# Performance work log

Hardware: AMD Instinct MI355X
Metric: run time of the kernel (lower is better)

## Reference

```python
import jax, jax.numpy as jnp
import numpy as np

B, C, H, W, K, NCLASS = 8, 512, 96, 96, 32, 19
EPS = 1e-5


def setup_inputs() -> dict:
    key = jax.random.key(0)
    ks = jax.random.split(key, 10)
    return {
        "x": jax.random.normal(ks[0], (B, C, H, W), dtype=jnp.float32),
        "conv_w": jax.random.normal(ks[1], (C, C), dtype=jnp.float32) * (1.0 / np.sqrt(C)),
        "bn2_w": jax.random.uniform(ks[2], (C,), dtype=jnp.float32, minval=0.5, maxval=1.5),
        "bn2_b": jax.random.normal(ks[3], (C,), dtype=jnp.float32) * 0.1,
        "bn2_mean": jnp.zeros((C,), jnp.float32),
        "bn2_var": jnp.ones((C,), jnp.float32),
        "codewords": jax.random.normal(ks[4], (K, C), dtype=jnp.float32) * (1.0 / np.sqrt(C)),
        "scale": jax.random.uniform(ks[5], (K,), dtype=jnp.float32, minval=-1.0, maxval=0.0),
        "bn1_w": jax.random.uniform(ks[6], (K,), dtype=jnp.float32, minval=0.5, maxval=1.5),
        "bn1_b": jax.random.normal(ks[7], (K,), dtype=jnp.float32) * 0.1,
        "bn1_mean": jnp.zeros((K,), jnp.float32),
        "bn1_var": jnp.ones((K,), jnp.float32),
        "fc_w": jax.random.normal(ks[8], (C, C), dtype=jnp.float32) * (1.0 / np.sqrt(C)),
        "fc_b": jnp.zeros((C,), jnp.float32),
        "se_w": jax.random.normal(ks[9], (NCLASS, C), dtype=jnp.float32) * (1.0 / np.sqrt(C)),
        "se_b": jnp.zeros((NCLASS,), jnp.float32),
    }


def reference(x, conv_w, bn2_w, bn2_b, bn2_mean, bn2_var,
              codewords, scale, bn1_w, bn1_b, bn1_mean, bn1_var,
              fc_w, fc_b, se_w, se_b):
    # 1x1 conv (no bias) + BN2d (inference) + ReLU
    h = jnp.einsum('oc,bchw->bohw', conv_w, x)
    s2 = bn2_w / jnp.sqrt(bn2_var + EPS)
    h = jax.nn.relu(h * s2[None, :, None, None]
                    + (bn2_b - bn2_mean * s2)[None, :, None, None])

    # Encoding: soft assignment over K codewords
    X = h.reshape(B, C, H * W).transpose(0, 2, 1)       # (B, N, C)
    x2 = jnp.sum(X * X, axis=-1)                        # (B, N)
    c2 = jnp.sum(codewords * codewords, axis=-1)        # (K,)
    xc = jnp.einsum('bnd,kd->bnk', X, codewords)        # (B, N, K)
    sl = scale[None, None, :] * (x2[:, :, None] - 2.0 * xc + c2[None, None, :])
    A = jax.nn.softmax(sl, axis=-1)                     # (B, N, K)
    # E[b,k,d] = sum_n A[b,n,k] * (X[b,n,d] - codewords[k,d])
    E = (jnp.einsum('bnk,bnd->bkd', A, X)
         - jnp.sum(A, axis=1)[:, :, None] * codewords[None, :, :])  # (B, K, C)

    # BN1d over the K channel dim (inference) + ReLU + mean over K
    s1 = bn1_w / jnp.sqrt(bn1_var + EPS)
    E = jax.nn.relu(E * s1[None, :, None] + (bn1_b - bn1_mean * s1)[None, :, None])
    en = jnp.mean(E, axis=1)                            # (B, C)

    # SE-style gate
    gamma = jax.nn.sigmoid(en @ fc_w.T + fc_b)          # (B, C)
    out = jax.nn.relu(x + x * gamma[:, :, None, None])  # (B, C, H, W)
    se = en @ se_w.T + se_b                             # (B, NCLASS)
    return (out, se)
```

## Files before the change

### kernel.cpp

```cpp
#include <hip/hip_runtime.h>
#include <math.h>

#define EPSV 1e-5f

typedef __attribute__((ext_vector_type(8))) short short8;
typedef __attribute__((ext_vector_type(4))) float f32x4;

namespace {
constexpr int NB=8, C=512, NPIX=9216, K=32, NCLS=19;

constexpr size_t o_WB    = 0;
constexpr size_t o_CWB   = 131072;
constexpr size_t o_A2    = 139264;
constexpr size_t o_B2    = 139776;
constexpr size_t o_C2    = 140288;
constexpr size_t o_X2    = 140320;
constexpr size_t o_EW    = 214048;
constexpr size_t o_ACNT  = 345120;
constexpr size_t o_EN    = 345376;
constexpr size_t o_GAMMA = 349472;
constexpr size_t o_XT    = 353568;
constexpr size_t o_EPART = 19227936;
constexpr size_t WS_NEED = o_EPART*4 + (size_t)1152*16384*2;

constexpr int NPARTS_B = 144;
constexpr int FUSED_LDS = 78592;
}

__device__ __forceinline__ ushort f2bf(float f){
  unsigned u = __float_as_uint(f);
  return (ushort)((u + 0x7FFFu + ((u>>16)&1u)) >> 16);
}
__device__ __forceinline__ float bf2f(ushort h){
  return __uint_as_float(((unsigned)h)<<16);
}

__global__ __launch_bounds__(256) void k_prep(
    const float* __restrict__ convw, ushort* __restrict__ Wb,
    const float* __restrict__ cw,    ushort* __restrict__ cwb,
    const float* __restrict__ bn2w, const float* __restrict__ bn2b,
    const float* __restrict__ bn2m, const float* __restrict__ bn2v,
    float* __restrict__ pa, float* __restrict__ pb, float* __restrict__ c2g)
{
  const int bid = blockIdx.x, t = threadIdx.x;
  if (bid < 136){
    const float* src = (bid < 128) ? convw : cw;
    ushort* dst      = (bid < 128) ? Wb    : cwb;
    const int base   = (bid < 128) ? bid   : (bid - 128);
    int i = (base*256 + t)*8;
    float4 a = *(const float4*)(src+i), b = *(const float4*)(src+i+4);
    uint4 o;
    o.x = f2bf(a.x) | ((unsigned)f2bf(a.y)<<16);
    o.y = f2bf(a.z) | ((unsigned)f2bf(a.w)<<16);
    o.z = f2bf(b.x) | ((unsigned)f2bf(b.y)<<16);
    o.w = f2bf(b.z) | ((unsigned)f2bf(b.w)<<16);
    *(uint4*)(dst+i) = o;
  } else {
    for (int o = t; o < C; o += 256){
      float s = bn2w[o] * rsqrtf(bn2v[o] + EPSV);
      pa[o] = s;
      pb[o] = bn2b[o] - bn2m[o] * s;
    }
    int kk = t>>3, part = t&7;
    float s = 0.f;
    for (int c = part*64; c < part*64 + 64; c += 4){
      float4 w = *(const float4*)(cw + kk*512 + c);
      s += w.x*w.x + w.y*w.y + w.z*w.z + w.w*w.w;
    }
    s += __shfl_xor(s, 1);
    s += __shfl_xor(s, 2);
    s += __shfl_xor(s, 4);
    if (part == 0) c2g[kk] = s;
  }
}

__global__ __launch_bounds__(256) void k_T(const float* __restrict__ x,
                                           ushort* __restrict__ xT){
  __shared__ float xs[64*68];
  const int bid = blockIdx.x;
  const int ct = bid & 7;
  const int nt = bid >> 3;
  const int b = nt / 144, ntl = nt % 144;
  const int c0 = ct*64, n0 = ntl*64;
  const int t = threadIdx.x;
  const float* src = x + ((size_t)b*C + c0)*NPIX + n0;
#pragma unroll
  for (int p = 0; p < 4; ++p){
    const int cr = p*16 + (t>>4);
    const int nc = (t&15)*4;
    *(float4*)(xs + cr*68 + nc) = *(const float4*)(src + (size_t)cr*NPIX + nc);
  }
  __syncthreads();
  const int nr = t>>2, ck = (t&3)*16;
  uint pk[8];
#pragma unroll
  for (int j = 0; j < 8; ++j){
    float f0 = xs[(ck + 2*j  )*68 + nr];
    float f1 = xs[(ck + 2*j+1)*68 + nr];
    pk[j] = (uint)f2bf(f0) | ((uint)f2bf(f1)<<16);
  }
  ushort* dst = xT + ((size_t)(b*NPIX + n0 + nr))*512 + c0 + ck;
  *(uint4*)(dst)   = make_uint4(pk[0],pk[1],pk[2],pk[3]);
  *(uint4*)(dst+8) = make_uint4(pk[4],pk[5],pk[6],pk[7]);
}

__global__ __launch_bounds__(256,2) void k_fused(
  const ushort* __restrict__ Wb, const ushort* __restrict__ xT,
  const ushort* __restrict__ cwb,
  const float* __restrict__ pA2, const float* __restrict__ pB2,
  const float* __restrict__ scale, const float* __restrict__ c2g,
  ushort* __restrict__ Epart, float* __restrict__ EwAtomic,
  float* __restrict__ Acnt, int useAtomic)
{
  extern __shared__ char smem[];
  ushort* As  = (ushort*)smem;
  ushort* Bs  = As + 512*64;
  ushort* hs  = (ushort*)smem;
  ushort* Pl  = (ushort*)(smem + 73728);
  float*  x2s = (float*)(smem + 78336);

  const int t = threadIdx.x, bid = blockIdx.x;
  const int wave = t>>6, lane = t&63;
  const int lg = lane>>4, l15 = lane&15;
  const int b = bid / NPARTS_B;
  const size_t n0 = (size_t)bid * 64;

  if (t < 64) x2s[t] = 0.f;

  f32x4 acc[8][4];
#pragma unroll
  for (int mi = 0; mi < 8; ++mi)
#pragma unroll
    for (int nj = 0; nj < 4; ++nj) acc[mi][nj] = (f32x4){0.f,0.f,0.f,0.f};

  const int srow = t>>3, sq = t&7;
  for (int s = 0; s < 8; ++s) {
    const int c0 = s*64;
    __syncthreads();
#pragma unroll
    for (int p = 0; p < 16; ++p) {
      const int r = p*32 + srow;
      uint4 v = *(const uint4*)(Wb + r*512 + c0 + sq*8);
      *(uint4*)(As + r*64 + (((sq ^ (r&7))&7)<<3)) = v;
    }
#pragma unroll
    for (int p = 0; p < 2; ++p) {
      const int r = p*32 + srow;
      uint4 v = *(const uint4*)(xT + (n0+r)*512 + c0 + sq*8);
      *(uint4*)(Bs + r*64 + (((sq ^ (r&7))&7)<<3)) = v;
    }
    __syncthreads();
#pragma unroll
    for (int kk = 0; kk < 2; ++kk) {
      short8 af[8], bfv[4];
#pragma unroll
      for (int mi = 0; mi < 8; ++mi) {
        const int r = wave*128 + mi*16 + l15;
        af[mi] = *(const short8*)(As + r*64 + ((((kk*4+lg) ^ (r&7))&7)<<3));
      }
#pragma unroll
      for (int nj = 0; nj < 4; ++nj) {
        const int r = nj*16 + l15;
        bfv[nj] = *(const short8*)(Bs + r*64 + ((((kk*4+lg) ^ (r&7))&7)<<3));
      }
#pragma unroll
      for (int mi = 0; mi < 8; ++mi)
#pragma unroll
        for (int nj = 0; nj < 4; ++nj)
          acc[mi][nj] = __builtin_amdgcn_mfma_f32_16x16x32_bf16(af[mi], bfv[nj], acc[mi][nj], 0,0,0);
    }
  }
  __syncthreads();

  float x2p[4] = {0.f,0.f,0.f,0.f};
#pragma unroll
  for (int mi = 0; mi < 8; ++mi) {
    const int ob = wave*128 + mi*16 + lg*4;
    const float4 sa = *(const float4*)(pA2 + ob);
    const float4 sb = *(const float4*)(pB2 + ob);
#pragma unroll
    for (int nj = 0; nj < 4; ++nj) {
      const int px = nj*16 + l15;
      f32x4 a = acc[mi][nj];
      float h0 = fmaxf(fmaf(a[0], sa.x, sb.x), 0.f);
      float h1 = fmaxf(fmaf(a[1], sa.y, sb.y), 0.f);
      float h2 = fmaxf(fmaf(a[2], sa.z, sb.z), 0.f);
      float h3 = fmaxf(fmaf(a[3], sa.w, sb.w), 0.f);
      uint2 pk;
      pk.x = f2bf(h0) | ((unsigned)f2bf(h1)<<16);
      pk.y = f2bf(h2) | ((unsigned)f2bf(h3)<<16);
      *(uint2*)(hs + px*520 + ob) = pk;
      h0 = bf2f((ushort)(pk.x & 0xFFFFu)); h1 = bf2f((ushort)(pk.x >> 16));
      h2 = bf2f((ushort)(pk.y & 0xFFFFu)); h3 = bf2f((ushort)(pk.y >> 16));
      x2p[nj] += h0*h0 + h1*h1 + h2*h2 + h3*h3;
    }
  }
#pragma unroll
  for (int nj = 0; nj < 4; ++nj) {
    float v = x2p[nj];
    v += __shfl_xor(v, 16);
    v += __shfl_xor(v, 32);
    if (lg == 0) atomicAdd(&x2s[nj*16 + l15], v);
  }
  __syncthreads();

  float sc[2][4], cv[2][4];
#pragma unroll
  for (int f=0; f<2; ++f)
#pragma unroll
    for (int i=0; i<4; ++i){
      int k = f*16 + lg*4 + i;
      sc[f][i] = scale[k];
      cv[f][i] = c2g[k];
    }

  f32x4 xacc[2];
  xacc[0] = (f32x4){0.f,0.f,0.f,0.f};
  xacc[1] = (f32x4){0.f,0.f,0.f,0.f};
  {
    const ushort* hrow  = hs + (wave*16 + l15)*520 + lg*8;
    const ushort* arow0 = cwb + (l15)*512 + lg*8;
    const ushort* arow1 = cwb + (16 + l15)*512 + lg*8;
#pragma unroll
    for (int s = 0; s < 16; ++s){
      short8 bfr = *(const short8*)(hrow  + s*32);
      short8 a0  = *(const short8*)(arow0 + s*32);
      short8 a1  = *(const short8*)(arow1 + s*32);
      xacc[0] = __builtin_amdgcn_mfma_f32_16x16x32_bf16(a0, bfr, xacc[0], 0,0,0);
      xacc[1] = __builtin_amdgcn_mfma_f32_16x16x32_bf16(a1, bfr, xacc[1], 0,0,0);
    }
  }
  const float x2v = x2s[wave*16 + l15];
  float sl[2][4];
  float mx = -1e30f;
#pragma unroll
  for (int f=0; f<2; ++f)
#pragma unroll
    for (int i=0; i<4; ++i){
      sl[f][i] = sc[f][i]*(x2v - 2.f*xacc[f][i] + cv[f][i]);
      mx = fmaxf(mx, sl[f][i]);
    }
  mx = fmaxf(mx, __shfl_xor(mx, 16));
  mx = fmaxf(mx, __shfl_xor(mx, 32));
  float pv[2][4];
  float ssum = 0.f;
#pragma unroll
  for (int f=0; f<2; ++f)
#pragma unroll
    for (int i=0; i<4; ++i){
      pv[f][i] = __expf(sl[f][i] - mx);
      ssum += pv[f][i];
    }
  ssum += __shfl_xor(ssum, 16);
  ssum += __shfl_xor(ssum, 32);
  const float inv = 1.f/ssum;
  float acs[2][4];
#pragma unroll
  for (int f=0; f<2; ++f)
#pragma unroll
    for (int i=0; i<4; ++i){
      float p = pv[f][i]*inv;
      ushort pb = f2bf(p);
      acs[f][i] = bf2f(pb);
      Pl[(f*16 + lg*4 + i)*72 + wave*16 + l15] = pb;
    }
  uint4 treg[16];
  {
    const ushort* src = hs + lane*520 + wave*128;
#pragma unroll
    for (int i=0; i<16; ++i) treg[i] = *(const uint4*)(src + i*8);
  }
  __syncthreads();
  {
    ushort* dstT = hs + (size_t)(wave*128)*72 + lane;
#pragma unroll
    for (int i=0; i<16; ++i){
      uint4 v = treg[i];
#pragma unroll
      for (int w2=0; w2<4; ++w2){
        unsigned word = (&v.x)[w2];
        dstT[(i*8 + w2*2    )*72] = (ushort)(word & 0xFFFFu);
        dstT[(i*8 + w2*2 + 1)*72] = (ushort)(word >> 16);
      }
    }
  }
  __syncthreads();
  f32x4 Eacc[2][8];
#pragma unroll
  for (int f=0; f<2; ++f)
#pragma unroll
    for (int nf=0; nf<8; ++nf) Eacc[f][nf] = (f32x4){0.f,0.f,0.f,0.f};
  short8 pa[2][2];
#pragma unroll
  for (int f=0; f<2; ++f)
#pragma unroll
    for (int ks=0; ks<2; ++ks)
      pa[f][ks] = *(const short8*)(Pl + (f*16 + l15)*72 + ks*32 + lg*8);
#pragma unroll
  for (int nf=0; nf<8; ++nf){
    const ushort* brow = hs + (size_t)(wave*128 + nf*16 + l15)*72 + lg*8;
    short8 b0 = *(const short8*)(brow);
    short8 b1 = *(const short8*)(brow + 32);
    Eacc[0][nf] = __builtin_amdgcn_mfma_f32_16x16x32_bf16(pa[0][0], b0, Eacc[0][nf], 0,0,0);
    Eacc[0][nf] = __builtin_amdgcn_mfma_f32_16x16x32_bf16(pa[0][1], b1, Eacc[0][nf], 0,0,0);
    Eacc[1][nf] = __builtin_amdgcn_mfma_f32_16x16x32_bf16(pa[1][0], b0, Eacc[1][nf], 0,0,0);
    Eacc[1][nf] = __builtin_amdgcn_mfma_f32_16x16x32_bf16(pa[1][1], b1, Eacc[1][nf], 0,0,0);
  }

  if (!useAtomic){
    ushort* pbase = Epart + (size_t)bid*16384;
#pragma unroll
    for (int f=0; f<2; ++f)
#pragma unroll
      for (int nf=0; nf<8; ++nf){
        const int c = wave*128 + nf*16 + l15;
        f32x4 a = Eacc[f][nf];
        uint2 pk;
        pk.x = f2bf(a[0]) | ((unsigned)f2bf(a[1])<<16);
        pk.y = f2bf(a[2]) | ((unsigned)f2bf(a[3])<<16);
        *(uint2*)(pbase + (size_t)c*32 + f*16 + lg*4) = pk;
      }
  } else {
    float* pbase = EwAtomic + (size_t)b*16384;
#pragma unroll
    for (int f=0; f<2; ++f)
#pragma unroll
      for (int nf=0; nf<8; ++nf){
        const int c = wave*128 + nf*16 + l15;
        float* p = pbase + (size_t)c*32 + f*16 + lg*4;
        atomicAdd(p+0, Eacc[f][nf][0]);
        atomicAdd(p+1, Eacc[f][nf][1]);
        atomicAdd(p+2, Eacc[f][nf][2]);
        atomicAdd(p+3, Eacc[f][nf][3]);
      }
  }
#pragma unroll
  for (int f=0; f<2; ++f)
#pragma unroll
    for (int i=0; i<4; ++i){
      float v = acs[f][i];
      v += __shfl_xor(v, 1);
      v += __shfl_xor(v, 2);
      v += __shfl_xor(v, 4);
      v += __shfl_xor(v, 8);
      if (l15 == 0) atomicAdd(&Acnt[b*32 + f*16 + lg*4 + i], v);
    }
}

__global__ __launch_bounds__(256) void k_en2(
    const ushort* __restrict__ Epart, const float* __restrict__ EwAtomic,
    const float* __restrict__ Acnt, const float* __restrict__ cw,
    const float* __restrict__ bn1w, const float* __restrict__ bn1b,
    const float* __restrict__ bn1m, const float* __restrict__ bn1v,
    float* __restrict__ en, int useAtomic)
{
  const int b = blockIdx.x >> 6;
  const int cchunk = blockIdx.x & 63;
  const int t = threadIdx.x;
  const int c_local = t >> 5, k = t & 31;
  const int c = cchunk*8 + c_local;

  float acc = 0.f;
  if (!useAtomic){
    const ushort* base = Epart + (size_t)b*NPARTS_B*16384 + cchunk*256 + t;
    for (int g = 0; g < NPARTS_B; ++g)
      acc += bf2f(base[(size_t)g*16384]);
  } else {
    acc = EwAtomic[(size_t)b*16384 + (size_t)c*32 + k];
  }
  float s1 = bn1w[k]*rsqrtf(bn1v[k]+EPSV);
  float t1 = bn1b[k] - bn1m[k]*s1;
  float e = acc - Acnt[b*32 + k]*cw[(size_t)k*512 + c];
  float v = fmaxf(fmaf(e, s1, t1), 0.f);
  v += __shfl_xor(v, 1);
  v += __shfl_xor(v, 2);
  v += __shfl_xor(v, 4);
  v += __shfl_xor(v, 8);
  v += __shfl_xor(v, 16);
  if (k == 0) en[(size_t)b*512 + c] = v*(1.f/32.f);
}

__global__ __launch_bounds__(512) void k_gate(
    const float* __restrict__ en, const float* __restrict__ fcw,
    const float* __restrict__ fcb, const float* __restrict__ sew,
    const float* __restrict__ seb, float* __restrict__ gamma,
    float* __restrict__ se_out)
{
    __shared__ float es[C];
    const int b = blockIdx.x;
    es[threadIdx.x] = en[(size_t)b * C + threadIdx.x];
    __syncthreads();
    {
        const int c = threadIdx.x;
        float z = fcb[c];
        const float* wr = fcw + (size_t)c * C;
        for (int i = 0; i < C; i += 4) {
            const float4 w = *(const float4*)(wr + i);
            z += w.x * es[i] + w.y * es[i + 1] + w.z * es[i + 2] + w.w * es[i + 3];
        }
        gamma[(size_t)b * C + c] = 1.f / (1.f + expf(-z));
    }
    if (threadIdx.x < NCLS * 8) {
        const int j = threadIdx.x >> 3, lane = threadIdx.x & 7;
        float p = 0.f;
        const float* swr = sew + (size_t)j * C;
        for (int i = lane * 64; i < lane * 64 + 64; i += 4) {
            const float4 w = *(const float4*)(swr + i);
            p += w.x * es[i] + w.y * es[i + 1] + w.z * es[i + 2] + w.w * es[i + 3];
        }
        p += __shfl_xor(p, 1);
        p += __shfl_xor(p, 2);
        p += __shfl_xor(p, 4);
        if (lane == 0) se_out[b * NCLS + j] = p + seb[j];
    }
}

__global__ __launch_bounds__(256) void k_out(
    const float* __restrict__ x, const float* __restrict__ gamma,
    float* __restrict__ out)
{
    const int total4 = NB * C * NPIX / 4;
    for (int i = blockIdx.x * blockDim.x + threadIdx.x; i < total4;
         i += gridDim.x * blockDim.x) {
        const int flat = i * 4;
        const int bc = flat / NPIX;
        const float gsc = 1.f + gamma[bc];
        float4 v = *(const float4*)(x + flat);
        v.x = fmaxf(v.x * gsc, 0.f);
        v.y = fmaxf(v.y * gsc, 0.f);
        v.z = fmaxf(v.z * gsc, 0.f);
        v.w = fmaxf(v.w * gsc, 0.f);
        *(float4*)(out + flat) = v;
    }
}

extern "C" void kernel_launch(void* const* d_in, const int* in_sizes, int n_in,
                              void* d_out, int out_size, void* d_ws, size_t ws_size,
                              hipStream_t stream)
{
    const float* x     = (const float*)d_in[0];
    const float* convw = (const float*)d_in[1];
    const float* bn2w  = (const float*)d_in[2];
    const float* bn2b  = (const float*)d_in[3];
    const float* bn2m  = (const float*)d_in[4];
    const float* bn2v  = (const float*)d_in[5];
    const float* cw    = (const float*)d_in[6];
    const float* scale = (const float*)d_in[7];
    const float* bn1w  = (const float*)d_in[8];
    const float* bn1b  = (const float*)d_in[9];
    const float* bn1m  = (const float*)d_in[10];
    const float* bn1v  = (const float*)d_in[11];
    const float* fcw   = (const float*)d_in[12];
    const float* fcb   = (const float*)d_in[13];
    const float* sew   = (const float*)d_in[14];
    const float* seb   = (const float*)d_in[15];

    float* ws = (float*)d_ws;
    float* out = (float*)d_out;
    float* se_out = out + (size_t)NB * C * NPIX;

    ushort* Wb    = (ushort*)(ws + o_WB);
    ushort* cwb   = (ushort*)(ws + o_CWB);
    ushort* xT    = (ushort*)(ws + o_XT);
    ushort* Epart = (ushort*)(ws + o_EPART);

    const bool use_part = ws_size >= WS_NEED;
    const int useAtomic = use_part ? 0 : 1;

    (void)hipFuncSetAttribute((const void*)k_fused,
                              hipFuncAttributeMaxDynamicSharedMemorySize, FUSED_LDS);

    hipMemsetAsync(ws + o_EW, 0, (size_t)(NB*C*K + 256) * sizeof(float), stream);

    k_prep<<<137, 256, 0, stream>>>(convw, Wb, cw, cwb,
                                    bn2w, bn2b, bn2m, bn2v,
                                    ws + o_A2, ws + o_B2, ws + o_C2);
    k_T<<<9216, 256, 0, stream>>>(x, xT);
    k_fused<<<1152, 256, FUSED_LDS, stream>>>(Wb, xT, cwb,
                                              ws + o_A2, ws + o_B2,
                                              scale, ws + o_C2,
                                              Epart, ws + o_EW, ws + o_ACNT, useAtomic);
    k_en2<<<512, 256, 0, stream>>>(Epart, ws + o_EW, ws + o_ACNT, cw,
                                   bn1w, bn1b, bn1m, bn1v, ws + o_EN, useAtomic);
    k_gate<<<8, 512, 0, stream>>>(ws + o_EN, fcw, fcb, sew, seb,
                                  ws + o_GAMMA, se_out);
    k_out<<<2048, 256, 0, stream>>>(x, ws + o_GAMMA, out);
}
```

Measured before the change: 329.9 us.

## Split fused encoding kernel into two 32-pixel sub-tiles to raise occupancy

The fused conv+encoding kernel now handles its 64 pixels as two sequential 32-pixel sub-tiles with a 32-wide K step. This shrinks LDS from about 78KB to 50KB and the accumulator register footprint, so launch bounds can target 3 blocks per CU. Softmax is restructured through an LDS score buffer, and assignment counts are reduced in LDS before one global atomic per codeword. The trade-off is twice the W tile reloads, more barriers per block, and a bf16 read-modify-write of the partial E output between sub-tiles, which adds rounding error.

```diff
diff --git a/kernel.cpp b/kernel.cpp
--- a/kernel.cpp
+++ b/kernel.cpp
@@ -24,7 +24,7 @@
 constexpr size_t WS_NEED = o_EPART*4 + (size_t)1152*16384*2;
 
 constexpr int NPARTS_B = 144;
-constexpr int FUSED_LDS = 78592;
+constexpr int FUSED_LDS = 50432;
 }
 
 __device__ __forceinline__ ushort f2bf(float f){
@@ -104,7 +104,7 @@
   *(uint4*)(dst+8) = make_uint4(pk[4],pk[5],pk[6],pk[7]);
 }
 
-__global__ __launch_bounds__(256,2) void k_fused(
+__global__ __launch_bounds__(256,3) void k_fused(
   const ushort* __restrict__ Wb, const ushort* __restrict__ xT,
   const ushort* __restrict__ cwb,
   const float* __restrict__ pA2, const float* __restrict__ pB2,
@@ -114,237 +114,222 @@
 {
   extern __shared__ char smem[];
   ushort* As  = (ushort*)smem;
-  ushort* Bs  = As + 512*64;
   ushort* hs  = (ushort*)smem;
-  ushort* Pl  = (ushort*)(smem + 73728);
-  float*  x2s = (float*)(smem + 78336);
+  ushort* hsT = (ushort*)smem;
+  ushort* Bs  = (ushort*)(smem + 40960);
+  float*  Sl  = (float*) (smem + 43008);
+  ushort* Pl  = (ushort*)(smem + 47616);
+  float*  x2s = (float*) (smem + 50176);
+  float*  acnt= (float*) (smem + 50304);
 
   const int t = threadIdx.x, bid = blockIdx.x;
-  const int wave = t>>6, lane = t&63;
-  const int lg = lane>>4, l15 = lane&15;
+  const int wave = t>>6, lane = t&63, lg = lane>>4, l15 = lane&15;
   const int b = bid / NPARTS_B;
-  const size_t n0 = (size_t)bid * 64;
-
-  if (t < 64) x2s[t] = 0.f;
-
-  f32x4 acc[8][4];
-#pragma unroll
-  for (int mi = 0; mi < 8; ++mi)
-#pragma unroll
-    for (int nj = 0; nj < 4; ++nj) acc[mi][nj] = (f32x4){0.f,0.f,0.f,0.f};
-
-  const int srow = t>>3, sq = t&7;
-  for (int s = 0; s < 8; ++s) {
-    const int c0 = s*64;
+  const int f_  = wave >> 1;
+  const int png = wave & 1;
+  const int sr = t>>2, sq = t&3;
+
+  if (t < 32) acnt[t] = 0.f;
+
+  float sck[4], cvk[4];
+#pragma unroll
+  for (int i = 0; i < 4; ++i){
+    const int k = f_*16 + lg*4 + i;
+    sck[i] = scale[k];
+    cvk[i] = c2g[k];
+  }
+
+  for (int st = 0; st < 2; ++st){
+    const size_t n0 = (size_t)bid*64 + st*32;
+    if (t < 32) x2s[t] = 0.f;
+
+    f32x4 acc[8][2];
+#pragma unroll
+    for (int mi = 0; mi < 8; ++mi){
+      acc[mi][0] = (f32x4){0.f,0.f,0.f,0.f};
+      acc[mi][1] = (f32x4){0.f,0.f,0.f,0.f};
+    }
+    for (int s = 0; s < 16; ++s){
+      const int c0 = s*32;
+      __syncthreads();
+#pragma unroll
+      for (int p = 0; p < 8; ++p){
+        const int r = p*64 + sr;
+        uint4 v = *(const uint4*)(Wb + r*512 + c0 + sq*8);
+        *(uint4*)(As + r*32 + (((sq ^ ((r>>1)&3))&3)<<3)) = v;
+      }
+      if (t < 128){
+        const int r = sr;
+        uint4 v = *(const uint4*)(xT + (n0+r)*512 + c0 + sq*8);
+        *(uint4*)(Bs + r*32 + (((sq ^ ((r>>1)&3))&3)<<3)) = v;
+      }
+      __syncthreads();
+      short8 af[8], bf2[2];
+#pragma unroll
+      for (int mi = 0; mi < 8; ++mi){
+        const int r = wave*128 + mi*16 + l15;
+        af[mi] = *(const short8*)(As + r*32 + (((lg ^ ((r>>1)&3))&3)<<3));
+      }
+#pragma unroll
+      for (int nj = 0; nj < 2; ++nj){
+        const int r = nj*16 + l15;
+        bf2[nj] = *(const short8*)(Bs + r*32 + (((lg ^ ((r>>1)&3))&3)<<3));
+      }
+#pragma unroll
+      for (int mi = 0; mi < 8; ++mi){
+        acc[mi][0] = __builtin_amdgcn_mfma_f32_16x16x32_bf16(af[mi], bf2[0], acc[mi][0], 0,0,0);
+        acc[mi][1] = __builtin_amdgcn_mfma_f32_16x16x32_bf16(af[mi], bf2[1], acc[mi][1], 0,0,0);
+      }
+    }
     __syncthreads();
-#pragma unroll
-    for (int p = 0; p < 16; ++p) {
-      const int r = p*32 + srow;
-      uint4 v = *(const uint4*)(Wb + r*512 + c0 + sq*8);
-      *(uint4*)(As + r*64 + (((sq ^ (r&7))&7)<<3)) = v;
-    }
-#pragma unroll
-    for (int p = 0; p < 2; ++p) {
-      const int r = p*32 + srow;
-      uint4 v = *(const uint4*)(xT + (n0+r)*512 + c0 + sq*8);
-      *(uint4*)(Bs + r*64 + (((sq ^ (r&7))&7)<<3)) = v;
+
+    float x2p0 = 0.f, x2p1 = 0.f;
+#pragma unroll
+    for (int mi = 0; mi < 8; ++mi){
+      const int ob = wave*128 + mi*16 + lg*4;
+      const float4 sa = *(const float4*)(pA2 + ob);
+      const float4 sb = *(const float4*)(pB2 + ob);
+#pragma unroll
+      for (int nj = 0; nj < 2; ++nj){
+        const int px = nj*16 + l15;
+        f32x4 a = acc[mi][nj];
+        float h0 = fmaxf(fmaf(a[0], sa.x, sb.x), 0.f);
+        float h1 = fmaxf(fmaf(a[1], sa.y, sb.y), 0.f);
+        float h2 = fmaxf(fmaf(a[2], sa.z, sb.z), 0.f);
+        float h3 = fmaxf(fmaf(a[3], sa.w, sb.w), 0.f);
+        uint2 pk;
+        pk.x = f2bf(h0) | ((unsigned)f2bf(h1)<<16);
+        pk.y = f2bf(h2) | ((unsigned)f2bf(h3)<<16);
+        *(uint2*)(hs + px*520 + ob) = pk;
+        float g0 = bf2f((ushort)(pk.x & 0xFFFFu)), g1 = bf2f((ushort)(pk.x >> 16));
+        float g2 = bf2f((ushort)(pk.y & 0xFFFFu)), g3 = bf2f((ushort)(pk.y >> 16));
+        float sqr = g0*g0 + g1*g1 + g2*g2 + g3*g3;
+        if (nj == 0) x2p0 += sqr; else x2p1 += sqr;
+      }
+    }
+    {
+      float v = x2p0;
+      v += __shfl_xor(v, 16); v += __shfl_xor(v, 32);
+      if (lg == 0) atomicAdd(&x2s[l15], v);
+      v = x2p1;
+      v += __shfl_xor(v, 16); v += __shfl_xor(v, 32);
+      if (lg == 0) atomicAdd(&x2s[16 + l15], v);
     }
     __syncthreads();
-#pragma unroll
-    for (int kk = 0; kk < 2; ++kk) {
-      short8 af[8], bfv[4];
-#pragma unroll
-      for (int mi = 0; mi < 8; ++mi) {
-        const int r = wave*128 + mi*16 + l15;
-        af[mi] = *(const short8*)(As + r*64 + ((((kk*4+lg) ^ (r&7))&7)<<3));
-      }
-#pragma unroll
-      for (int nj = 0; nj < 4; ++nj) {
-        const int r = nj*16 + l15;
-        bfv[nj] = *(const short8*)(Bs + r*64 + ((((kk*4+lg) ^ (r&7))&7)<<3));
-      }
-#pragma unroll
-      for (int mi = 0; mi < 8; ++mi)
-#pragma unroll
-        for (int nj = 0; nj < 4; ++nj)
-          acc[mi][nj] = __builtin_amdgcn_mfma_f32_16x16x32_bf16(af[mi], bfv[nj], acc[mi][nj], 0,0,0);
-    }
-  }
-  __syncthreads();
-
-  float x2p[4] = {0.f,0.f,0.f,0.f};
-#pragma unroll
-  for (int mi = 0; mi < 8; ++mi) {
-    const int ob = wave*128 + mi*16 + lg*4;
-    const float4 sa = *(const float4*)(pA2 + ob);
-    const float4 sb = *(const float4*)(pB2 + ob);
-#pragma unroll
-    for (int nj = 0; nj < 4; ++nj) {
-      const int px = nj*16 + l15;
-      f32x4 a = acc[mi][nj];
-      float h0 = fmaxf(fmaf(a[0], sa.x, sb.x), 0.f);
-      float h1 = fmaxf(fmaf(a[1], sa.y, sb.y), 0.f);
-      float h2 = fmaxf(fmaf(a[2], sa.z, sb.z), 0.f);
-      float h3 = fmaxf(fmaf(a[3], sa.w, sb.w), 0.f);
-      uint2 pk;
-      pk.x = f2bf(h0) | ((unsigned)f2bf(h1)<<16);
-      pk.y = f2bf(h2) | ((unsigned)f2bf(h3)<<16);
-      *(uint2*)(hs + px*520 + ob) = pk;
-      h0 = bf2f((ushort)(pk.x & 0xFFFFu)); h1 = bf2f((ushort)(pk.x >> 16));
-      h2 = bf2f((ushort)(pk.y & 0xFFFFu)); h3 = bf2f((ushort)(pk.y >> 16));
-      x2p[nj] += h0*h0 + h1*h1 + h2*h2 + h3*h3;
-    }
-  }
-#pragma unroll
-  for (int nj = 0; nj < 4; ++nj) {
-    float v = x2p[nj];
-    v += __shfl_xor(v, 16);
-    v += __shfl_xor(v, 32);
-    if (lg == 0) atomicAdd(&x2s[nj*16 + l15], v);
-  }
-  __syncthreads();
-
-  float sc[2][4], cv[2][4];
-#pragma unroll
-  for (int f=0; f<2; ++f)
-#pragma unroll
-    for (int i=0; i<4; ++i){
-      int k = f*16 + lg*4 + i;
-      sc[f][i] = scale[k];
-      cv[f][i] = c2g[k];
-    }
-
-  f32x4 xacc[2];
-  xacc[0] = (f32x4){0.f,0.f,0.f,0.f};
-  xacc[1] = (f32x4){0.f,0.f,0.f,0.f};
-  {
-    const ushort* hrow  = hs + (wave*16 + l15)*520 + lg*8;
-    const ushort* arow0 = cwb + (l15)*512 + lg*8;
-    const ushort* arow1 = cwb + (16 + l15)*512 + lg*8;
-#pragma unroll
-    for (int s = 0; s < 16; ++s){
-      short8 bfr = *(const short8*)(hrow  + s*32);
-      short8 a0  = *(const short8*)(arow0 + s*32);
-      short8 a1  = *(const short8*)(arow1 + s*32);
-      xacc[0] = __builtin_amdgcn_mfma_f32_16x16x32_bf16(a0, bfr, xacc[0], 0,0,0);
-      xacc[1] = __builtin_amdgcn_mfma_f32_16x16x32_bf16(a1, bfr, xacc[1], 0,0,0);
-    }
-  }
-  const float x2v = x2s[wave*16 + l15];
-  float sl[2][4];
-  float mx = -1e30f;
-#pragma unroll
-  for (int f=0; f<2; ++f)
-#pragma unroll
-    for (int i=0; i<4; ++i){
-      sl[f][i] = sc[f][i]*(x2v - 2.f*xacc[f][i] + cv[f][i]);
-      mx = fmaxf(mx, sl[f][i]);
-    }
-  mx = fmaxf(mx, __shfl_xor(mx, 16));
-  mx = fmaxf(mx, __shfl_xor(mx, 32));
-  float pv[2][4];
-  float ssum = 0.f;
-#pragma unroll
-  for (int f=0; f<2; ++f)
-#pragma unroll
-    for (int i=0; i<4; ++i){
-      pv[f][i] = __expf(sl[f][i] - mx);
-      ssum += pv[f][i];
-    }
-  ssum += __shfl_xor(ssum, 16);
-  ssum += __shfl_xor(ssum, 32);
-  const float inv = 1.f/ssum;
-  float acs[2][4];
-#pragma unroll
-  for (int f=0; f<2; ++f)
-#pragma unroll
-    for (int i=0; i<4; ++i){
-      float p = pv[f][i]*inv;
-      ushort pb = f2bf(p);
-      acs[f][i] = bf2f(pb);
-      Pl[(f*16 + lg*4 + i)*72 + wave*16 + l15] = pb;
-    }
-  uint4 treg[16];
-  {
-    const ushort* src = hs + lane*520 + wave*128;
-#pragma unroll
-    for (int i=0; i<16; ++i) treg[i] = *(const uint4*)(src + i*8);
-  }
-  __syncthreads();
-  {
-    ushort* dstT = hs + (size_t)(wave*128)*72 + lane;
-#pragma unroll
-    for (int i=0; i<16; ++i){
-      uint4 v = treg[i];
-#pragma unroll
-      for (int w2=0; w2<4; ++w2){
-        unsigned word = (&v.x)[w2];
-        dstT[(i*8 + w2*2    )*72] = (ushort)(word & 0xFFFFu);
-        dstT[(i*8 + w2*2 + 1)*72] = (ushort)(word >> 16);
-      }
-    }
-  }
-  __syncthreads();
-  f32x4 Eacc[2][8];
-#pragma unroll
-  for (int f=0; f<2; ++f)
-#pragma unroll
-    for (int nf=0; nf<8; ++nf) Eacc[f][nf] = (f32x4){0.f,0.f,0.f,0.f};
-  short8 pa[2][2];
-#pragma unroll
-  for (int f=0; f<2; ++f)
-#pragma unroll
-    for (int ks=0; ks<2; ++ks)
-      pa[f][ks] = *(const short8*)(Pl + (f*16 + l15)*72 + ks*32 + lg*8);
-#pragma unroll
-  for (int nf=0; nf<8; ++nf){
-    const ushort* brow = hs + (size_t)(wave*128 + nf*16 + l15)*72 + lg*8;
-    short8 b0 = *(const short8*)(brow);
-    short8 b1 = *(const short8*)(brow + 32);
-    Eacc[0][nf] = __builtin_amdgcn_mfma_f32_16x16x32_bf16(pa[0][0], b0, Eacc[0][nf], 0,0,0);
-    Eacc[0][nf] = __builtin_amdgcn_mfma_f32_16x16x32_bf16(pa[0][1], b1, Eacc[0][nf], 0,0,0);
-    Eacc[1][nf] = __builtin_amdgcn_mfma_f32_16x16x32_bf16(pa[1][0], b0, Eacc[1][nf], 0,0,0);
-    Eacc[1][nf] = __builtin_amdgcn_mfma_f32_16x16x32_bf16(pa[1][1], b1, Eacc[1][nf], 0,0,0);
-  }
-
-  if (!useAtomic){
-    ushort* pbase = Epart + (size_t)bid*16384;
-#pragma unroll
-    for (int f=0; f<2; ++f)
-#pragma unroll
-      for (int nf=0; nf<8; ++nf){
-        const int c = wave*128 + nf*16 + l15;
-        f32x4 a = Eacc[f][nf];
-        uint2 pk;
-        pk.x = f2bf(a[0]) | ((unsigned)f2bf(a[1])<<16);
-        pk.y = f2bf(a[2]) | ((unsigned)f2bf(a[3])<<16);
-        *(uint2*)(pbase + (size_t)c*32 + f*16 + lg*4) = pk;
-      }
-  } else {
-    float* pbase = EwAtomic + (size_t)b*16384;
-#pragma unroll
-    for (int f=0; f<2; ++f)
-#pragma unroll
-      for (int nf=0; nf<8; ++nf){
-        const int c = wave*128 + nf*16 + l15;
-        float* p = pbase + (size_t)c*32 + f*16 + lg*4;
-        atomicAdd(p+0, Eacc[f][nf][0]);
-        atomicAdd(p+1, Eacc[f][nf][1]);
-        atomicAdd(p+2, Eacc[f][nf][2]);
-        atomicAdd(p+3, Eacc[f][nf][3]);
-      }
-  }
-#pragma unroll
-  for (int f=0; f<2; ++f)
-#pragma unroll
-    for (int i=0; i<4; ++i){
-      float v = acs[f][i];
-      v += __shfl_xor(v, 1);
-      v += __shfl_xor(v, 2);
-      v += __shfl_xor(v, 4);
-      v += __shfl_xor(v, 8);
-      if (l15 == 0) atomicAdd(&Acnt[b*32 + f*16 + lg*4 + i], v);
-    }
+
+    f32x4 xacc = (f32x4){0.f,0.f,0.f,0.f};
+    {
+      const ushort* arow = cwb + (size_t)(f_*16 + l15)*512 + lg*8;
+      const ushort* hrow = hs + (png*16 + l15)*520 + lg*8;
+#pragma unroll
+      for (int s = 0; s < 16; ++s)
+        xacc = __builtin_amdgcn_mfma_f32_16x16x32_bf16(
+            *(const short8*)(arow + s*32), *(const short8*)(hrow + s*32), xacc, 0,0,0);
+    }
+    {
+      const float x2v = x2s[png*16 + l15];
+#pragma unroll
+      for (int i = 0; i < 4; ++i)
+        Sl[(png*16 + l15)*36 + f_*16 + lg*4 + i] = sck[i]*(x2v - 2.f*xacc[i] + cvk[i]);
+    }
+    __syncthreads();
+
+    {
+      const int p = t>>3, j = t&7;
+      float4 v = *(const float4*)(Sl + p*36 + j*4);
+      float mx = fmaxf(fmaxf(v.x, v.y), fmaxf(v.z, v.w));
+      mx = fmaxf(mx, __shfl_xor(mx, 1));
+      mx = fmaxf(mx, __shfl_xor(mx, 2));
+      mx = fmaxf(mx, __shfl_xor(mx, 4));
+      v.x = __expf(v.x - mx); v.y = __expf(v.y - mx);
+      v.z = __expf(v.z - mx); v.w = __expf(v.w - mx);
+      float ssum = v.x + v.y + v.z + v.w;
+      ssum += __shfl_xor(ssum, 1);
+      ssum += __shfl_xor(ssum, 2);
+      ssum += __shfl_xor(ssum, 4);
+      const float inv = 1.f/ssum;
+      ushort p0 = f2bf(v.x*inv), p1 = f2bf(v.y*inv), p2 = f2bf(v.z*inv), p3 = f2bf(v.w*inv);
+      Pl[(j*4+0)*40 + p] = p0;  Pl[(j*4+1)*40 + p] = p1;
+      Pl[(j*4+2)*40 + p] = p2;  Pl[(j*4+3)*40 + p] = p3;
+      atomicAdd(&acnt[j*4+0], bf2f(p0));
+      atomicAdd(&acnt[j*4+1], bf2f(p1));
+      atomicAdd(&acnt[j*4+2], bf2f(p2));
+      atomicAdd(&acnt[j*4+3], bf2f(p3));
+    }
+    uint4 treg[8];
+    {
+      const int px_ = t&31, cb = (t>>5)*64;
+      const ushort* src = hs + px_*520 + cb;
+#pragma unroll
+      for (int i = 0; i < 8; ++i) treg[i] = *(const uint4*)(src + i*8);
+      __syncthreads();
+#pragma unroll
+      for (int i = 0; i < 8; ++i){
+        uint4 v = treg[i];
+#pragma unroll
+        for (int w2 = 0; w2 < 4; ++w2){
+          unsigned word = (&v.x)[w2];
+          hsT[(cb + i*8 + w2*2    )*40 + px_] = (ushort)(word & 0xFFFFu);
+          hsT[(cb + i*8 + w2*2 + 1)*40 + px_] = (ushort)(word >> 16);
+        }
+      }
+    }
+    __syncthreads();
+
+    f32x4 Eacc[2][8];
+#pragma unroll
+    for (int fi = 0; fi < 2; ++fi)
+#pragma unroll
+      for (int nf = 0; nf < 8; ++nf) Eacc[fi][nf] = (f32x4){0.f,0.f,0.f,0.f};
+    {
+      short8 pa0 = *(const short8*)(Pl + (l15)*40 + lg*8);
+      short8 pa1 = *(const short8*)(Pl + (16 + l15)*40 + lg*8);
+#pragma unroll
+      for (int nf = 0; nf < 8; ++nf){
+        const ushort* brow = hsT + (size_t)(wave*128 + nf*16 + l15)*40 + lg*8;
+        short8 bb = *(const short8*)(brow);
+        Eacc[0][nf] = __builtin_amdgcn_mfma_f32_16x16x32_bf16(pa0, bb, Eacc[0][nf], 0,0,0);
+        Eacc[1][nf] = __builtin_amdgcn_mfma_f32_16x16x32_bf16(pa1, bb, Eacc[1][nf], 0,0,0);
+      }
+    }
+    if (!useAtomic){
+      ushort* pbase = Epart + (size_t)bid*16384;
+#pragma unroll
+      for (int fi = 0; fi < 2; ++fi)
+#pragma unroll
+        for (int nf = 0; nf < 8; ++nf){
+          const int c = wave*128 + nf*16 + l15;
+          ushort* addr = pbase + (size_t)c*32 + fi*16 + lg*4;
+          f32x4 e = Eacc[fi][nf];
+          if (st == 1){
+            uint2 old = *(const uint2*)(addr);
+            e[0] += bf2f((ushort)(old.x & 0xFFFFu));
+            e[1] += bf2f((ushort)(old.x >> 16));
+            e[2] += bf2f((ushort)(old.y & 0xFFFFu));
+            e[3] += bf2f((ushort)(old.y >> 16));
+          }
+          uint2 pk;
+          pk.x = f2bf(e[0]) | ((unsigned)f2bf(e[1])<<16);
+          pk.y = f2bf(e[2]) | ((unsigned)f2bf(e[3])<<16);
+          *(uint2*)(addr) = pk;
+        }
+    } else {
+      float* pbase = EwAtomic + (size_t)b*16384;
+#pragma unroll
+      for (int fi = 0; fi < 2; ++fi)
+#pragma unroll
+        for (int nf = 0; nf < 8; ++nf){
+          const int c = wave*128 + nf*16 + l15;
+          float* p = pbase + (size_t)c*32 + fi*16 + lg*4;
+          atomicAdd(p+0, Eacc[fi][nf][0]);
+          atomicAdd(p+1, Eacc[fi][nf][1]);
+          atomicAdd(p+2, Eacc[fi][nf][2]);
+          atomicAdd(p+3, Eacc[fi][nf][3]);
+        }
+    }
+  }
+
+  if (t < 32) atomicAdd(&Acnt[b*32 + t], acnt[t]);
 }
 
 __global__ __launch_bounds__(256) void k_en2(
```

After: 943.3 us. +185.9%, slower.

## Fuse x transpose and bf16 conversion into the fused GEMM tile load

Applied to the files above, without the earlier changes.

Removes the separate transpose kernel that wrote a bf16 channel-last copy of x to workspace. The fused kernel now reads fp32 x directly in its native layout, converts it to bf16 and scatters it into the swizzled LDS B tile. This removes one full write and read of a roughly 75MB intermediate plus a kernel launch. In exchange it adds scalar 2-byte LDS stores with possible bank conflicts and doubles the global bytes read per B tile inside the GEMM loop.

```diff
diff --git a/kernel.cpp b/kernel.cpp
--- a/kernel.cpp
+++ b/kernel.cpp
@@ -14,12 +14,10 @@
 constexpr size_t o_A2    = 139264;
 constexpr size_t o_B2    = 139776;
 constexpr size_t o_C2    = 140288;
-constexpr size_t o_X2    = 140320;
 constexpr size_t o_EW    = 214048;
 constexpr size_t o_ACNT  = 345120;
 constexpr size_t o_EN    = 345376;
 constexpr size_t o_GAMMA = 349472;
-constexpr size_t o_XT    = 353568;
 constexpr size_t o_EPART = 19227936;
 constexpr size_t WS_NEED = o_EPART*4 + (size_t)1152*16384*2;
 
@@ -74,38 +72,8 @@
   }
 }
 
-__global__ __launch_bounds__(256) void k_T(const float* __restrict__ x,
-                                           ushort* __restrict__ xT){
-  __shared__ float xs[64*68];
-  const int bid = blockIdx.x;
-  const int ct = bid & 7;
-  const int nt = bid >> 3;
-  const int b = nt / 144, ntl = nt % 144;
-  const int c0 = ct*64, n0 = ntl*64;
-  const int t = threadIdx.x;
-  const float* src = x + ((size_t)b*C + c0)*NPIX + n0;
-#pragma unroll
-  for (int p = 0; p < 4; ++p){
-    const int cr = p*16 + (t>>4);
-    const int nc = (t&15)*4;
-    *(float4*)(xs + cr*68 + nc) = *(const float4*)(src + (size_t)cr*NPIX + nc);
-  }
-  __syncthreads();
-  const int nr = t>>2, ck = (t&3)*16;
-  uint pk[8];
-#pragma unroll
-  for (int j = 0; j < 8; ++j){
-    float f0 = xs[(ck + 2*j  )*68 + nr];
-    float f1 = xs[(ck + 2*j+1)*68 + nr];
-    pk[j] = (uint)f2bf(f0) | ((uint)f2bf(f1)<<16);
-  }
-  ushort* dst = xT + ((size_t)(b*NPIX + n0 + nr))*512 + c0 + ck;
-  *(uint4*)(dst)   = make_uint4(pk[0],pk[1],pk[2],pk[3]);
-  *(uint4*)(dst+8) = make_uint4(pk[4],pk[5],pk[6],pk[7]);
-}
-
 __global__ __launch_bounds__(256,2) void k_fused(
-  const ushort* __restrict__ Wb, const ushort* __restrict__ xT,
+  const ushort* __restrict__ Wb, const float* __restrict__ x,
   const ushort* __restrict__ cwb,
   const float* __restrict__ pA2, const float* __restrict__ pB2,
   const float* __restrict__ scale, const float* __restrict__ c2g,
@@ -123,7 +91,7 @@
   const int wave = t>>6, lane = t&63;
   const int lg = lane>>4, l15 = lane&15;
   const int b = bid / NPARTS_B;
-  const size_t n0 = (size_t)bid * 64;
+  const int np0 = (bid % NPARTS_B) * 64;
 
   if (t < 64) x2s[t] = 0.f;
 
@@ -134,6 +102,7 @@
     for (int nj = 0; nj < 4; ++nj) acc[mi][nj] = (f32x4){0.f,0.f,0.f,0.f};
 
   const int srow = t>>3, sq = t&7;
+  const int crB = t>>2, px0 = (t&3)*16;
   for (int s = 0; s < 8; ++s) {
     const int c0 = s*64;
     __syncthreads();
@@ -143,11 +112,20 @@
       uint4 v = *(const uint4*)(Wb + r*512 + c0 + sq*8);
       *(uint4*)(As + r*64 + (((sq ^ (r&7))&7)<<3)) = v;
     }
-#pragma unroll
-    for (int p = 0; p < 2; ++p) {
-      const int r = p*32 + srow;
-      uint4 v = *(const uint4*)(xT + (n0+r)*512 + c0 + sq*8);
-      *(uint4*)(Bs + r*64 + (((sq ^ (r&7))&7)<<3)) = v;
+    {
+      const float* xsrc = x + ((size_t)b*C + (c0 + crB))*NPIX + np0 + px0;
+      float4 w0 = *(const float4*)(xsrc);
+      float4 w1 = *(const float4*)(xsrc + 4);
+      float4 w2 = *(const float4*)(xsrc + 8);
+      float4 w3 = *(const float4*)(xsrc + 12);
+      const int sg = crB>>3, so = crB&7;
+      const float vals[16] = {w0.x,w0.y,w0.z,w0.w, w1.x,w1.y,w1.z,w1.w,
+                              w2.x,w2.y,w2.z,w2.w, w3.x,w3.y,w3.z,w3.w};
+#pragma unroll
+      for (int j = 0; j < 16; ++j){
+        const int px = px0 + j;
+        Bs[px*64 + (((sg ^ (px&7))&7)<<3) + so] = f2bf(vals[j]);
+      }
     }
     __syncthreads();
 #pragma unroll
@@ -461,7 +439,6 @@
 
     ushort* Wb    = (ushort*)(ws + o_WB);
     ushort* cwb   = (ushort*)(ws + o_CWB);
-    ushort* xT    = (ushort*)(ws + o_XT);
     ushort* Epart = (ushort*)(ws + o_EPART);
 
     const bool use_part = ws_size >= WS_NEED;
@@ -475,8 +452,7 @@
     k_prep<<<137, 256, 0, stream>>>(convw, Wb, cw, cwb,
                                     bn2w, bn2b, bn2m, bn2v,
                                     ws + o_A2, ws + o_B2, ws + o_C2);
-    k_T<<<9216, 256, 0, stream>>>(x, xT);
-    k_fused<<<1152, 256, FUSED_LDS, stream>>>(Wb, xT, cwb,
+    k_fused<<<1152, 256, FUSED_LDS, stream>>>(Wb, x, cwb,
                                               ws + o_A2, ws + o_B2,
                                               scale, ws + o_C2,
                                               Epart, ws + o_EW, ws + o_ACNT, useAtomic);
```

New measurement: 419.4 us. 1.27x slower.
